# Kernel tuning notes

Hardware: AMD Instinct MI355X
Metric: run time of the kernel (lower is better)

Reference implementation:

```python
import jax, jax.numpy as jnp
import numpy as np

B, K, N, F_IN, F_OUT, T = 8, 3, 2048, 16, 64, 12


def setup_inputs() -> dict:
    key = jax.random.key(0)
    k1, k2, k3, k4 = jax.random.split(key, 4)
    x = jax.random.normal(k1, (B, N, F_IN, T), dtype=jnp.float32)
    spatial_attention = jax.random.normal(k2, (B, K, N, N), dtype=jnp.float32)
    adj = jax.random.uniform(k3, (N, N), dtype=jnp.float32)  # fusiongraph() output
    Theta = jax.random.normal(k4, (K, F_IN, F_OUT), dtype=jnp.float32) * 0.1
    return {"x": x, "spatial_attention": spatial_attention, "adj": adj, "Theta": Theta}


def _cheb_polynomials(L_tilde, k_order):
    # NOTE: original uses ELEMENTWISE multiply in the recurrence (L_tilde * T_{k-1}),
    # faithfully reproduced here.
    n = L_tilde.shape[0]
    polys = [jnp.eye(n, dtype=L_tilde.dtype), L_tilde]
    for _ in range(2, k_order):
        polys.append(2.0 * L_tilde * polys[-1] - polys[-2])
    return jnp.stack(polys[:k_order], axis=0)  # (K, N, N)


def reference(x, spatial_attention, adj, Theta):
    # Unnormalized graph Laplacian L = D - A (torch_geometric get_laplacian default).
    deg = jnp.sum(adj, axis=1)                      # (N,)
    L_tilde = jnp.diag(deg) - adj                   # (N, N)
    cheb = _cheb_polynomials(L_tilde, K)            # (K, N, N)

    # softmax over dim=1 of each (B,N,N) slice -> axis=2 of (B,K,N,N); time-invariant.
    attn = jax.nn.softmax(spatial_attention, axis=2)  # (B, K, N, N)
    Tka = cheb[None, :, :, :] * attn                  # (B, K, N, N)

    # rhs[b,n,f,t] = sum_m Tka[b,k,m,n] * x[b,m,f,t]; out = rhs @ Theta_k, summed over k.
    out = jnp.einsum('bkmn,bmft,kfo->bnot', Tka, x, Theta)  # (B, N, F_OUT, T)
    return jax.nn.relu(out)
```

## Files before the change

### kernel.cpp

```cpp
#include <hip/hip_runtime.h>


#define NB 8
#define NN 2048
#define FT 192
#define BN 64
#define BM 64
#define LBM 72

typedef __attribute__((ext_vector_type(8))) short short8;
typedef __attribute__((ext_vector_type(4))) float f32x4;

__device__ __forceinline__ unsigned short bf16_rne(float f) {
  unsigned u = __float_as_uint(f);
  u += 0x7FFFu + ((u >> 16) & 1u);
  return (unsigned short)(u >> 16);
}

__device__ __forceinline__ void gload_lds16(const float* g, float* l) {
  __builtin_amdgcn_global_load_lds(
      (const __attribute__((address_space(1))) void*)g,
      (__attribute__((address_space(3))) void*)l, 16, 0, 0);
}

__global__ __launch_bounds__(256) void k_deg(const float* __restrict__ adj,
                                             float* __restrict__ deg) {
  const int row = blockIdx.x;
  const float* r = adj + (size_t)row * NN;
  float s = 0.f;
  for (int j = threadIdx.x; j < NN; j += 256) s += r[j];
  for (int off = 32; off; off >>= 1) s += __shfl_down(s, off, 64);
  __shared__ float ls[4];
  if ((threadIdx.x & 63) == 0) ls[threadIdx.x >> 6] = s;
  __syncthreads();
  if (threadIdx.x == 0) deg[row] = ls[0] + ls[1] + ls[2] + ls[3];
}

__global__ __launch_bounds__(192) void k_xt(const float* __restrict__ x,
                                            unsigned short* __restrict__ xT) {
  const int b = blockIdx.y, m0 = blockIdx.x * 32, ft = threadIdx.x;
  const float* src = x + (size_t)b * NN * FT + ft;
  uint4* dst = (uint4*)(xT + ((size_t)b * FT + ft) * NN + m0);
#pragma unroll
  for (int g = 0; g < 4; ++g) {
    unsigned u[4];
#pragma unroll
    for (int j = 0; j < 4; ++j) {
      float lo = src[(size_t)(m0 + g * 8 + 2 * j) * FT];
      float hi = src[(size_t)(m0 + g * 8 + 2 * j + 1) * FT];
      u[j] = (unsigned)bf16_rne(lo) | ((unsigned)bf16_rne(hi) << 16);
    }
    dst[g] = make_uint4(u[0], u[1], u[2], u[3]);
  }
}

__global__ __launch_bounds__(256) void k_z0(const float* __restrict__ Sall,
                                            float* __restrict__ z0P,
                                            float* __restrict__ diagE) {
  __shared__ float zs[16][64];
  const int n0 = blockIdx.x * 64, b = blockIdx.y, half = blockIdx.z;
  const int t = threadIdx.x, n4 = (t & 15) * 4, rg = t >> 4;
  const float* S0 = Sall + (size_t)b * 3 * NN * NN;
  float z0 = 0.f, z1 = 0.f, z2 = 0.f, z3 = 0.f;
  const int mstart = half * 1024;
#pragma unroll 4
  for (int mm = rg; mm < 1024; mm += 16) {
    const int m = mstart + mm;
    const float4 v = *(const float4*)(S0 + (size_t)m * NN + n0 + n4);
    const float e0 = __expf(v.x), e1 = __expf(v.y), e2 = __expf(v.z),
                e3 = __expf(v.w);
    z0 += e0; z1 += e1; z2 += e2; z3 += e3;
    const int d = m - (n0 + n4);
    if (d >= 0 && d < 4) {
      const float ee[4] = {e0, e1, e2, e3};
      diagE[b * NN + m] = ee[d];
    }
  }
  zs[rg][n4 + 0] = z0;
  zs[rg][n4 + 1] = z1;
  zs[rg][n4 + 2] = z2;
  zs[rg][n4 + 3] = z3;
  __syncthreads();
  if (t < 64) {
    float s = 0.f;
#pragma unroll
    for (int g = 0; g < 16; ++g) s += zs[g][t];
    z0P[((size_t)b * 2 + half) * NN + n0 + t] = s;
  }
}

template <bool ISK1>
__device__ __forceinline__ void pack_chunk(const float* SrawSh,
                                           const float4 av[4],
                                           const float* __restrict__ deg,
                                           unsigned short* PtDst, float zp[4],
                                           const int pmg, const int pn4,
                                           const bool dchunk, const int n0) {
  unsigned short pk[4][4];
#pragma unroll
  for (int r = 0; r < 4; ++r) {
    const float4 s = *(const float4*)&SrawSh[(pmg * 4 + r) * BN + pn4];
    const float se[4] = {s.x, s.y, s.z, s.w};
    const float aa[4] = {av[r].x, av[r].y, av[r].z, av[r].w};
#pragma unroll
    for (int j = 0; j < 4; ++j) {
      const float e = __expf(se[j]);
      zp[j] += e;
      float cc = ISK1 ? (-aa[j]) : (2.f * aa[j] * aa[j]);
      if (dchunk) {
        if (pmg * 4 + r == pn4 + j) {
          const float L = deg[n0 + pn4 + j] - aa[j];
          cc = ISK1 ? L : (2.f * L * L - 1.f);
        }
      }
      pk[r][j] = bf16_rne(e * cc);
    }
  }
#pragma unroll
  for (int j = 0; j < 4; ++j) {
    uint2 v;
    v.x = (unsigned)pk[0][j] | ((unsigned)pk[1][j] << 16);
    v.y = (unsigned)pk[2][j] | ((unsigned)pk[3][j] << 16);
    *(uint2*)&PtDst[(pn4 + j) * LBM + pmg * 4] = v;
  }
}

template <int MS>
__global__ __launch_bounds__(256, 2) void k_main(
    const float* __restrict__ Sall, const float* __restrict__ adj,
    const float* __restrict__ deg, const unsigned short* __restrict__ xT,
    float* __restrict__ rhsP, float* __restrict__ z12P) {
  static_assert(MS == 1 || MS == 2, "MS");
  constexpr int C = 32 / MS;
  __shared__ unsigned short Pt[2][BN * LBM];
  __shared__ float Sraw[BM * BN];
  __shared__ float Zred[16][BN];

  const int flat = blockIdx.x + 32 * (blockIdx.y + 2 * blockIdx.z);
  const int xcd = flat & 7;
  const int jj = flat >> 3;
  const int tile = xcd * 4 + (jj & 3);
  const int rest = jj >> 2;
  const int kk = rest & 1;
  const int t2 = rest >> 1;
  const int ms = t2 % MS;
  const int b = t2 / MS;

  const int n0 = tile * BN, mbase = ms * (C * BM);
  const int t = threadIdx.x, lane = t & 63, w = t >> 6;
  const int ln = lane & 15, quad = lane >> 4;
  const int pn4 = (t & 15) * 4, pmg = t >> 4;
  const float* S = Sall + (size_t)(b * 3 + 1 + kk) * NN * NN;
  const unsigned short* xb = xT + (size_t)b * FT * NN;

  const f32x4 zero4 = {0.f, 0.f, 0.f, 0.f};
  f32x4 acc[4][3];
#pragma unroll
  for (int i = 0; i < 4; ++i)
#pragma unroll
    for (int q = 0; q < 3; ++q) acc[i][q] = zero4;
  float zp[4] = {0.f, 0.f, 0.f, 0.f};

  const int srow = (w << 4) + (lane >> 4);
  const int scol = (lane & 15) << 2;
  float* const lbase = &Sraw[(w << 4) * BN];

  {
    const float* g = S + (size_t)(mbase + srow) * NN + n0 + scol;
#pragma unroll
    for (int j2 = 0; j2 < 4; ++j2)
      gload_lds16(g + (size_t)(j2 * 4) * NN, lbase + j2 * 4 * BN);
  }
  float4 av[4];
#pragma unroll
  for (int r = 0; r < 4; ++r)
    av[r] = *(const float4*)(adj + (size_t)(mbase + pmg * 4 + r) * NN + n0 + pn4);
  asm volatile("s_waitcnt vmcnt(0)" ::: "memory");
  __builtin_amdgcn_sched_barrier(0);
  if (kk == 0)
    pack_chunk<true>(Sraw, av, deg, Pt[0], zp, pmg, pn4, mbase == n0, n0);
  else
    pack_chunk<false>(Sraw, av, deg, Pt[0], zp, pmg, pn4, mbase == n0, n0);
  __syncthreads();

  for (int c = 0; c < C; ++c) {
    const int cur = c & 1;
    const bool more = (c + 1 < C);
    const int m0 = mbase + c * BM;

    short8 bfr[2][3];
#pragma unroll
    for (int ks2 = 0; ks2 < 2; ++ks2)
#pragma unroll
      for (int q = 0; q < 3; ++q)
        bfr[ks2][q] = *(const short8*)(xb + (size_t)(w * 48 + q * 16 + ln) * NN +
                                       m0 + ks2 * 32 + quad * 8);
    __builtin_amdgcn_sched_barrier(0);

    if (more) {
      const int mn = m0 + BM;
      const float* g = S + (size_t)(mn + srow) * NN + n0 + scol;
#pragma unroll
      for (int j2 = 0; j2 < 4; ++j2)
        gload_lds16(g + (size_t)(j2 * 4) * NN, lbase + j2 * 4 * BN);
#pragma unroll
      for (int r = 0; r < 4; ++r)
        av[r] =
            *(const float4*)(adj + (size_t)(mn + pmg * 4 + r) * NN + n0 + pn4);
    }
    __builtin_amdgcn_sched_barrier(0);

#pragma unroll
    for (int ks2 = 0; ks2 < 2; ++ks2) {
      short8 af[4];
#pragma unroll
      for (int i = 0; i < 4; ++i)
        af[i] = *(const short8*)&Pt[cur][(i * 16 + ln) * LBM + ks2 * 32 +
                                         quad * 8];
#pragma unroll
      for (int i = 0; i < 4; ++i)
#pragma unroll
        for (int q = 0; q < 3; ++q)
          acc[i][q] = __builtin_amdgcn_mfma_f32_16x16x32_bf16(
              af[i], bfr[ks2][q], acc[i][q], 0, 0, 0);
    }

    if (more) {
      asm volatile("s_waitcnt vmcnt(0)" ::: "memory");
      __builtin_amdgcn_sched_barrier(0);
      const bool dch = (m0 + BM == n0);
      if (kk == 0)
        pack_chunk<true>(Sraw, av, deg, Pt[cur ^ 1], zp, pmg, pn4, dch, n0);
      else
        pack_chunk<false>(Sraw, av, deg, Pt[cur ^ 1], zp, pmg, pn4, dch, n0);
    }
    __syncthreads();
  }

#pragma unroll
  for (int j = 0; j < 4; ++j) Zred[pmg][pn4 + j] = zp[j];
  __syncthreads();
  if (t < 64) {
    float Z = 0.f;
#pragma unroll
    for (int g = 0; g < 16; ++g) Z += Zred[g][t];
    z12P[((size_t)(kk * 8 + b) * MS + ms) * NN + n0 + t] = Z;
  }

  float* outp = rhsP + (((size_t)(kk * 8 + b) * MS + ms) * NN + n0) * FT;
#pragma unroll
  for (int i = 0; i < 4; ++i)
#pragma unroll
    for (int q = 0; q < 3; ++q) {
      const int ft = w * 48 + q * 16 + ln;
#pragma unroll
      for (int r = 0; r < 4; ++r) {
        const int nl = i * 16 + quad * 4 + r;
        outp[(size_t)nl * FT + ft] = acc[i][q][r];
      }
    }
}

__global__ __launch_bounds__(256) void k_out(
    const float* __restrict__ x, const float* __restrict__ Theta,
    const float* __restrict__ rhsP, const float* __restrict__ z12P,
    const float* __restrict__ z0P, const float* __restrict__ diagE,
    float* __restrict__ out, int MS) {
  __shared__ float xs[4][FT], r1s[4][FT], r2s[4][FT];
  __shared__ float sc[3][4];
  const int b = blockIdx.y, n0 = blockIdx.x * 4;
  const int t = threadIdx.x, o = t & 63, nl = t >> 6;

  for (int l = t; l < 576; l += 256) {
    const int arr = l / 192, idx = l - arr * 192;
    const int row = idx / 48, c4 = (idx % 48) * 4;
    if (arr == 0) {
      *(float4*)&xs[row][c4] =
          *(const float4*)(x + ((size_t)b * NN + n0 + row) * FT + c4);
    } else {
      float4 s = {0.f, 0.f, 0.f, 0.f};
      for (int ms = 0; ms < MS; ++ms) {
        const float4 v = *(const float4*)(rhsP +
            (((size_t)((arr - 1) * 8 + b) * MS + ms) * NN + n0 + row) * FT +
            c4);
        s.x += v.x; s.y += v.y; s.z += v.z; s.w += v.w;
      }
      float* dstbase = (arr == 1) ? &r1s[0][0] : &r2s[0][0];
      *(float4*)(dstbase + row * FT + c4) = s;
    }
  }
  if (t < 12) {
    const int j = t & 3, which = t >> 2;
    float v;
    if (which < 2) {
      float z = 0.f;
      for (int ms = 0; ms < MS; ++ms)
        z += z12P[((size_t)(which * 8 + b) * MS + ms) * NN + n0 + j];
      v = 1.f / z;
    } else {
      float z = 0.f;
      for (int q = 0; q < 2; ++q) z += z0P[((size_t)b * 2 + q) * NN + n0 + j];
      v = diagE[b * NN + n0 + j] / z;
    }
    sc[which][j] = v;
  }
  __syncthreads();

  float a0[12], a1[12], a2[12];
#pragma unroll
  for (int tt = 0; tt < 12; ++tt) a0[tt] = a1[tt] = a2[tt] = 0.f;
#pragma unroll
  for (int f = 0; f < 16; ++f) {
    const float th0 = Theta[(0 * 16 + f) * 64 + o];
    const float th1 = Theta[(1 * 16 + f) * 64 + o];
    const float th2 = Theta[(2 * 16 + f) * 64 + o];
#pragma unroll
    for (int tt = 0; tt < 12; ++tt) {
      a0[tt] += th0 * xs[nl][f * 12 + tt];
      a1[tt] += th1 * r1s[nl][f * 12 + tt];
      a2[tt] += th2 * r2s[nl][f * 12 + tt];
    }
  }
  const float rz1 = sc[0][nl], rz2 = sc[1][nl], c0 = sc[2][nl];
  float r[12];
#pragma unroll
  for (int tt = 0; tt < 12; ++tt)
    r[tt] = fmaxf(a0[tt] * c0 + a1[tt] * rz1 + a2[tt] * rz2, 0.f);
  float4* op4 = (float4*)(out + (((size_t)b * NN + n0 + nl) * 64 + o) * 12);
  op4[0] = make_float4(r[0], r[1], r[2], r[3]);
  op4[1] = make_float4(r[4], r[5], r[6], r[7]);
  op4[2] = make_float4(r[8], r[9], r[10], r[11]);
}

extern "C" void kernel_launch(void* const* d_in, const int* in_sizes, int n_in,
                              void* d_out, int out_size, void* d_ws,
                              size_t ws_size, hipStream_t stream) {
  const float* x = (const float*)d_in[0];
  const float* s_attn = (const float*)d_in[1];
  const float* adj = (const float*)d_in[2];
  const float* Theta = (const float*)d_in[3];
  float* out = (float*)d_out;
  char* ws = (char*)d_ws;

  const size_t szXT = (size_t)NB * FT * NN * 2;
  const size_t szDeg = NN * 4;
  const size_t szZ0 = (size_t)NB * 2 * NN * 4;
  const size_t szDiag = (size_t)NB * NN * 4;
  const size_t base = szXT + szDeg + szZ0 + szDiag;
  const size_t perMS = (size_t)2 * NB * NN * 4
                       + (size_t)2 * NB * NN * FT * 4;

  int MS = 0;
  if (ws_size >= base + 2 * perMS) MS = 2;
  else if (ws_size >= base + 1 * perMS) MS = 1;
  if (MS == 0) return;

  unsigned short* xT = (unsigned short*)ws;
  float* deg = (float*)(ws + szXT);
  float* z0P = (float*)(ws + szXT + szDeg);
  float* diagE = (float*)(ws + szXT + szDeg + szZ0);
  float* z12P = (float*)(ws + base);
  float* rhsP = (float*)(ws + base + (size_t)2 * NB * MS * NN * 4);

  hipLaunchKernelGGL(k_deg, dim3(NN), dim3(256), 0, stream, adj, deg);
  hipLaunchKernelGGL(k_xt, dim3(64, NB), dim3(192), 0, stream, x, xT);
  hipLaunchKernelGGL(k_z0, dim3(32, NB, 2), dim3(256), 0, stream, s_attn, z0P,
                     diagE);
  if (MS == 2) {
    hipLaunchKernelGGL(k_main<2>, dim3(32, 2, NB * 2), dim3(256), 0, stream,
                       s_attn, adj, deg, xT, rhsP, z12P);
  } else {
    hipLaunchKernelGGL(k_main<1>, dim3(32, 2, NB * 1), dim3(256), 0, stream,
                       s_attn, adj, deg, xT, rhsP, z12P);
  }
  hipLaunchKernelGGL(k_out, dim3(512, NB), dim3(256), 0, stream, x, Theta,
                     rhsP, z12P, z0P, diagE, out, MS);
}
```

Before: 654.7 us.

## Fuse softmax-normalizer, both Chebyshev GEMMs and Theta epilogue into one kernel

Merges k_z0, k_main (both k=1 and k=2 branches, no M-split) and k_out into a single kernel per (batch, 32-column tile). Each block streams all three attention slices, computes the column softmax sums and diagonal term inline, runs two MFMA accumulations sharing the x fragments, and applies Theta, scaling and ReLU from LDS. This removes the partial rhs/z round trips through global memory, two launches and a redundant reread of x fragments. In exchange the grid shrinks to 512 blocks with a halved N tile, using more LDS per block and a serial full-M loop, which may lower occupancy and parallelism.

```diff
diff --git a/kernel.cpp b/kernel.cpp
--- a/kernel.cpp
+++ b/kernel.cpp
@@ -4,9 +4,10 @@
 #define NB 8
 #define NN 2048
 #define FT 192
-#define BN 64
+#define BN 32
 #define BM 64
 #define LBM 72
+#define ZST 33
 
 typedef __attribute__((ext_vector_type(8))) short short8;
 typedef __attribute__((ext_vector_type(4))) float f32x4;
@@ -54,287 +55,266 @@
   }
 }
 
-__global__ __launch_bounds__(256) void k_z0(const float* __restrict__ Sall,
-                                            float* __restrict__ z0P,
-                                            float* __restrict__ diagE) {
-  __shared__ float zs[16][64];
-  const int n0 = blockIdx.x * 64, b = blockIdx.y, half = blockIdx.z;
-  const int t = threadIdx.x, n4 = (t & 15) * 4, rg = t >> 4;
-  const float* S0 = Sall + (size_t)b * 3 * NN * NN;
-  float z0 = 0.f, z1 = 0.f, z2 = 0.f, z3 = 0.f;
-  const int mstart = half * 1024;
-#pragma unroll 4
-  for (int mm = rg; mm < 1024; mm += 16) {
-    const int m = mstart + mm;
-    const float4 v = *(const float4*)(S0 + (size_t)m * NN + n0 + n4);
-    const float e0 = __expf(v.x), e1 = __expf(v.y), e2 = __expf(v.z),
-                e3 = __expf(v.w);
-    z0 += e0; z1 += e1; z2 += e2; z3 += e3;
-    const int d = m - (n0 + n4);
-    if (d >= 0 && d < 4) {
-      const float ee[4] = {e0, e1, e2, e3};
-      diagE[b * NN + m] = ee[d];
-    }
-  }
-  zs[rg][n4 + 0] = z0;
-  zs[rg][n4 + 1] = z1;
-  zs[rg][n4 + 2] = z2;
-  zs[rg][n4 + 3] = z3;
-  __syncthreads();
-  if (t < 64) {
-    float s = 0.f;
-#pragma unroll
-    for (int g = 0; g < 16; ++g) s += zs[g][t];
-    z0P[((size_t)b * 2 + half) * NN + n0 + t] = s;
-  }
-}
-
-template <bool ISK1>
-__device__ __forceinline__ void pack_chunk(const float* SrawSh,
-                                           const float4 av[4],
-                                           const float* __restrict__ deg,
-                                           unsigned short* PtDst, float zp[4],
-                                           const int pmg, const int pn4,
-                                           const bool dchunk, const int n0) {
-  unsigned short pk[4][4];
-#pragma unroll
-  for (int r = 0; r < 4; ++r) {
-    const float4 s = *(const float4*)&SrawSh[(pmg * 4 + r) * BN + pn4];
-    const float se[4] = {s.x, s.y, s.z, s.w};
-    const float aa[4] = {av[r].x, av[r].y, av[r].z, av[r].w};
-#pragma unroll
-    for (int j = 0; j < 4; ++j) {
-      const float e = __expf(se[j]);
-      zp[j] += e;
-      float cc = ISK1 ? (-aa[j]) : (2.f * aa[j] * aa[j]);
-      if (dchunk) {
-        if (pmg * 4 + r == pn4 + j) {
-          const float L = deg[n0 + pn4 + j] - aa[j];
-          cc = ISK1 ? L : (2.f * L * L - 1.f);
-        }
-      }
-      pk[r][j] = bf16_rne(e * cc);
-    }
-  }
-#pragma unroll
-  for (int j = 0; j < 4; ++j) {
-    uint2 v;
-    v.x = (unsigned)pk[0][j] | ((unsigned)pk[1][j] << 16);
-    v.y = (unsigned)pk[2][j] | ((unsigned)pk[3][j] << 16);
-    *(uint2*)&PtDst[(pn4 + j) * LBM + pmg * 4] = v;
-  }
-}
-
-template <int MS>
-__global__ __launch_bounds__(256, 2) void k_main(
+__global__ __launch_bounds__(256, 2) void k_fused(
     const float* __restrict__ Sall, const float* __restrict__ adj,
     const float* __restrict__ deg, const unsigned short* __restrict__ xT,
-    float* __restrict__ rhsP, float* __restrict__ z12P) {
-  static_assert(MS == 1 || MS == 2, "MS");
-  constexpr int C = 32 / MS;
-  __shared__ unsigned short Pt[2][BN * LBM];
-  __shared__ float Sraw[BM * BN];
-  __shared__ float Zred[16][BN];
-
-  const int flat = blockIdx.x + 32 * (blockIdx.y + 2 * blockIdx.z);
-  const int xcd = flat & 7;
-  const int jj = flat >> 3;
-  const int tile = xcd * 4 + (jj & 3);
-  const int rest = jj >> 2;
-  const int kk = rest & 1;
-  const int t2 = rest >> 1;
-  const int ms = t2 % MS;
-  const int b = t2 / MS;
-
-  const int n0 = tile * BN, mbase = ms * (C * BM);
-  const int t = threadIdx.x, lane = t & 63, w = t >> 6;
+    const float* __restrict__ x, const float* __restrict__ Theta,
+    float* __restrict__ out) {
+  __shared__ __align__(16) char smem[74752];
+  __shared__ float dEs[BN];
+  __shared__ float sc[3][BN];
+
+  float* const Sr1 = (float*)smem;
+  float* const Sr2 = (float*)(smem + 8192);
+  unsigned short* const PtB = (unsigned short*)(smem + 16384);
+
+  const int flat = blockIdx.x + (blockIdx.y << 6);
+  const int b = flat & 7;
+  const int tile = flat >> 3;
+  const int n0 = tile * BN;
+
+  const int t = threadIdx.x;
+  const int lane = t & 63, w = t >> 6;
   const int ln = lane & 15, quad = lane >> 4;
-  const int pn4 = (t & 15) * 4, pmg = t >> 4;
-  const float* S = Sall + (size_t)(b * 3 + 1 + kk) * NN * NN;
+  const int col4 = (t & 7) << 2;
+  const int rowg = t >> 3;
+  const int srow = lane >> 3;
+  const int scol = (lane & 7) << 2;
+
+  const float* S0 = Sall + (size_t)b * 3 * NN * NN;
+  const float* S1 = S0 + (size_t)NN * NN;
+  const float* S2 = S1 + (size_t)NN * NN;
   const unsigned short* xb = xT + (size_t)b * FT * NN;
 
+  const int cdiag = n0 >> 6;
+  const float4 dgv = *(const float4*)(deg + n0 + col4);
+
   const f32x4 zero4 = {0.f, 0.f, 0.f, 0.f};
-  f32x4 acc[4][3];
-#pragma unroll
-  for (int i = 0; i < 4; ++i)
-#pragma unroll
-    for (int q = 0; q < 3; ++q) acc[i][q] = zero4;
-  float zp[4] = {0.f, 0.f, 0.f, 0.f};
-
-  const int srow = (w << 4) + (lane >> 4);
-  const int scol = (lane & 15) << 2;
-  float* const lbase = &Sraw[(w << 4) * BN];
-
+  f32x4 acc1[2][3], acc2[2][3];
+#pragma unroll
+  for (int i = 0; i < 2; ++i)
+#pragma unroll
+    for (int q = 0; q < 3; ++q) {
+      acc1[i][q] = zero4;
+      acc2[i][q] = zero4;
+    }
+  float zp0[4] = {0.f, 0.f, 0.f, 0.f};
+  float zp1[4] = {0.f, 0.f, 0.f, 0.f};
+  float zp2[4] = {0.f, 0.f, 0.f, 0.f};
+
+  auto STAGE = [&](int c) {
+    const int m0s = c * BM;
+#pragma unroll
+    for (int j2 = 0; j2 < 2; ++j2) {
+      const int r0 = (w << 4) + (j2 << 3);
+      const size_t go = (size_t)(m0s + r0 + srow) * NN + n0 + scol;
+      gload_lds16(S1 + go, Sr1 + r0 * BN);
+      gload_lds16(S2 + go, Sr2 + r0 * BN);
+    }
+  };
+
+  auto LOADAV = [&](int c, float4 av[2], float4 sv[2]) {
+#pragma unroll
+    for (int r = 0; r < 2; ++r) {
+      const int gm = c * BM + rowg * 2 + r;
+      av[r] = *(const float4*)(adj + (size_t)gm * NN + n0 + col4);
+      sv[r] = *(const float4*)(S0 + (size_t)gm * NN + n0 + col4);
+    }
+  };
+
+  auto PACK = [&](int c, int buf, const float4 av[2], const float4 sv[2]) {
+    const bool isd = (c == cdiag);
+    unsigned short* P1 = PtB + (size_t)buf * 2304;
+    unsigned short* P2 = PtB + (size_t)(2 + buf) * 2304;
+    unsigned short q1[2][4], q2[2][4];
+    const float dg[4] = {dgv.x, dgv.y, dgv.z, dgv.w};
+#pragma unroll
+    for (int r = 0; r < 2; ++r) {
+      const int lrow = rowg * 2 + r;
+      const float4 s1 = *(const float4*)&Sr1[lrow * BN + col4];
+      const float4 s2 = *(const float4*)&Sr2[lrow * BN + col4];
+      const float se1[4] = {s1.x, s1.y, s1.z, s1.w};
+      const float se2[4] = {s2.x, s2.y, s2.z, s2.w};
+      const float aa[4] = {av[r].x, av[r].y, av[r].z, av[r].w};
+      const float s0e[4] = {sv[r].x, sv[r].y, sv[r].z, sv[r].w};
+#pragma unroll
+      for (int j = 0; j < 4; ++j) {
+        const float e0 = __expf(s0e[j]);
+        const float e1 = __expf(se1[j]);
+        const float e2 = __expf(se2[j]);
+        zp0[j] += e0;
+        zp1[j] += e1;
+        zp2[j] += e2;
+        float c1 = -aa[j];
+        float c2 = 2.f * aa[j] * aa[j];
+        if (isd) {
+          if (c * BM + lrow == n0 + col4 + j) {
+            const float L = dg[j] - aa[j];
+            c1 = L;
+            c2 = 2.f * L * L - 1.f;
+            dEs[col4 + j] = e0;
+          }
+        }
+        q1[r][j] = bf16_rne(e1 * c1);
+        q2[r][j] = bf16_rne(e2 * c2);
+      }
+    }
+#pragma unroll
+    for (int j = 0; j < 4; ++j) {
+      const unsigned v1 = (unsigned)q1[0][j] | ((unsigned)q1[1][j] << 16);
+      const unsigned v2 = (unsigned)q2[0][j] | ((unsigned)q2[1][j] << 16);
+      *(unsigned*)&P1[(col4 + j) * LBM + rowg * 2] = v1;
+      *(unsigned*)&P2[(col4 + j) * LBM + rowg * 2] = v2;
+    }
+  };
+
+  STAGE(0);
   {
-    const float* g = S + (size_t)(mbase + srow) * NN + n0 + scol;
-#pragma unroll
-    for (int j2 = 0; j2 < 4; ++j2)
-      gload_lds16(g + (size_t)(j2 * 4) * NN, lbase + j2 * 4 * BN);
-  }
-  float4 av[4];
-#pragma unroll
-  for (int r = 0; r < 4; ++r)
-    av[r] = *(const float4*)(adj + (size_t)(mbase + pmg * 4 + r) * NN + n0 + pn4);
-  asm volatile("s_waitcnt vmcnt(0)" ::: "memory");
-  __builtin_amdgcn_sched_barrier(0);
-  if (kk == 0)
-    pack_chunk<true>(Sraw, av, deg, Pt[0], zp, pmg, pn4, mbase == n0, n0);
-  else
-    pack_chunk<false>(Sraw, av, deg, Pt[0], zp, pmg, pn4, mbase == n0, n0);
-  __syncthreads();
-
-  for (int c = 0; c < C; ++c) {
-    const int cur = c & 1;
-    const bool more = (c + 1 < C);
-    const int m0 = mbase + c * BM;
+    float4 av[2], sv[2];
+    LOADAV(0, av, sv);
+    asm volatile("s_waitcnt vmcnt(0)" ::: "memory");
+    __builtin_amdgcn_sched_barrier(0);
+    PACK(0, 0, av, sv);
+  }
+  __syncthreads();
+
+  for (int c = 0; c < 32; ++c) {
+    const int buf = c & 1;
+    const bool more = (c < 31);
+    const int m0 = c * BM;
 
     short8 bfr[2][3];
 #pragma unroll
     for (int ks2 = 0; ks2 < 2; ++ks2)
 #pragma unroll
       for (int q = 0; q < 3; ++q)
-        bfr[ks2][q] = *(const short8*)(xb + (size_t)(w * 48 + q * 16 + ln) * NN +
-                                       m0 + ks2 * 32 + quad * 8);
+        bfr[ks2][q] = *(const short8*)(xb +
+            (size_t)(w * 48 + q * 16 + ln) * NN + m0 + ks2 * 32 + quad * 8);
     __builtin_amdgcn_sched_barrier(0);
 
+    float4 avn[2], svn[2];
     if (more) {
-      const int mn = m0 + BM;
-      const float* g = S + (size_t)(mn + srow) * NN + n0 + scol;
-#pragma unroll
-      for (int j2 = 0; j2 < 4; ++j2)
-        gload_lds16(g + (size_t)(j2 * 4) * NN, lbase + j2 * 4 * BN);
-#pragma unroll
-      for (int r = 0; r < 4; ++r)
-        av[r] =
-            *(const float4*)(adj + (size_t)(mn + pmg * 4 + r) * NN + n0 + pn4);
+      STAGE(c + 1);
+      LOADAV(c + 1, avn, svn);
     }
     __builtin_amdgcn_sched_barrier(0);
 
 #pragma unroll
     for (int ks2 = 0; ks2 < 2; ++ks2) {
-      short8 af[4];
-#pragma unroll
-      for (int i = 0; i < 4; ++i)
-        af[i] = *(const short8*)&Pt[cur][(i * 16 + ln) * LBM + ks2 * 32 +
-                                         quad * 8];
-#pragma unroll
-      for (int i = 0; i < 4; ++i)
-#pragma unroll
-        for (int q = 0; q < 3; ++q)
-          acc[i][q] = __builtin_amdgcn_mfma_f32_16x16x32_bf16(
-              af[i], bfr[ks2][q], acc[i][q], 0, 0, 0);
+      short8 a1[2], a2[2];
+#pragma unroll
+      for (int i = 0; i < 2; ++i) {
+        a1[i] = *(const short8*)&PtB[(size_t)buf * 2304 + (i * 16 + ln) * LBM +
+                                     ks2 * 32 + quad * 8];
+        a2[i] = *(const short8*)&PtB[(size_t)(2 + buf) * 2304 +
+                                     (i * 16 + ln) * LBM + ks2 * 32 + quad * 8];
+      }
+#pragma unroll
+      for (int i = 0; i < 2; ++i)
+#pragma unroll
+        for (int q = 0; q < 3; ++q) {
+          acc1[i][q] = __builtin_amdgcn_mfma_f32_16x16x32_bf16(
+              a1[i], bfr[ks2][q], acc1[i][q], 0, 0, 0);
+          acc2[i][q] = __builtin_amdgcn_mfma_f32_16x16x32_bf16(
+              a2[i], bfr[ks2][q], acc2[i][q], 0, 0, 0);
+        }
     }
 
     if (more) {
       asm volatile("s_waitcnt vmcnt(0)" ::: "memory");
       __builtin_amdgcn_sched_barrier(0);
-      const bool dch = (m0 + BM == n0);
-      if (kk == 0)
-        pack_chunk<true>(Sraw, av, deg, Pt[cur ^ 1], zp, pmg, pn4, dch, n0);
-      else
-        pack_chunk<false>(Sraw, av, deg, Pt[cur ^ 1], zp, pmg, pn4, dch, n0);
+      PACK(c + 1, buf ^ 1, avn, svn);
     }
     __syncthreads();
   }
 
-#pragma unroll
-  for (int j = 0; j < 4; ++j) Zred[pmg][pn4 + j] = zp[j];
-  __syncthreads();
-  if (t < 64) {
+  float* Zr = (float*)smem;
+#pragma unroll
+  for (int j = 0; j < 4; ++j) {
+    Zr[0 * 32 * ZST + rowg * ZST + col4 + j] = zp0[j];
+    Zr[1 * 32 * ZST + rowg * ZST + col4 + j] = zp1[j];
+    Zr[2 * 32 * ZST + rowg * ZST + col4 + j] = zp2[j];
+  }
+  __syncthreads();
+  if (t < 96) {
+    const int which = t >> 5, n = t & 31;
     float Z = 0.f;
 #pragma unroll
-    for (int g = 0; g < 16; ++g) Z += Zred[g][t];
-    z12P[((size_t)(kk * 8 + b) * MS + ms) * NN + n0 + t] = Z;
-  }
-
-  float* outp = rhsP + (((size_t)(kk * 8 + b) * MS + ms) * NN + n0) * FT;
-#pragma unroll
-  for (int i = 0; i < 4; ++i)
+    for (int g = 0; g < 32; ++g) Z += Zr[which * 32 * ZST + g * ZST + n];
+    sc[which][n] = (which == 0) ? (dEs[n] / Z) : (1.f / Z);
+  }
+  __syncthreads();
+
+  float* const r1s = (float*)smem;
+  float* const r2s = (float*)(smem + 25088);
+  float* const xs = (float*)(smem + 50176);
+#pragma unroll
+  for (int i = 0; i < 2; ++i)
 #pragma unroll
     for (int q = 0; q < 3; ++q) {
       const int ft = w * 48 + q * 16 + ln;
 #pragma unroll
       for (int r = 0; r < 4; ++r) {
         const int nl = i * 16 + quad * 4 + r;
-        outp[(size_t)nl * FT + ft] = acc[i][q][r];
+        r1s[nl * 196 + ft] = acc1[i][q][r];
+        r2s[nl * 196 + ft] = acc2[i][q][r];
       }
     }
-}
-
-__global__ __launch_bounds__(256) void k_out(
-    const float* __restrict__ x, const float* __restrict__ Theta,
-    const float* __restrict__ rhsP, const float* __restrict__ z12P,
-    const float* __restrict__ z0P, const float* __restrict__ diagE,
-    float* __restrict__ out, int MS) {
-  __shared__ float xs[4][FT], r1s[4][FT], r2s[4][FT];
-  __shared__ float sc[3][4];
-  const int b = blockIdx.y, n0 = blockIdx.x * 4;
-  const int t = threadIdx.x, o = t & 63, nl = t >> 6;
-
-  for (int l = t; l < 576; l += 256) {
-    const int arr = l / 192, idx = l - arr * 192;
-    const int row = idx / 48, c4 = (idx % 48) * 4;
-    if (arr == 0) {
-      *(float4*)&xs[row][c4] =
-          *(const float4*)(x + ((size_t)b * NN + n0 + row) * FT + c4);
-    } else {
-      float4 s = {0.f, 0.f, 0.f, 0.f};
-      for (int ms = 0; ms < MS; ++ms) {
-        const float4 v = *(const float4*)(rhsP +
-            (((size_t)((arr - 1) * 8 + b) * MS + ms) * NN + n0 + row) * FT +
-            c4);
-        s.x += v.x; s.y += v.y; s.z += v.z; s.w += v.w;
-      }
-      float* dstbase = (arr == 1) ? &r1s[0][0] : &r2s[0][0];
-      *(float4*)(dstbase + row * FT + c4) = s;
-    }
-  }
-  if (t < 12) {
-    const int j = t & 3, which = t >> 2;
-    float v;
-    if (which < 2) {
-      float z = 0.f;
-      for (int ms = 0; ms < MS; ++ms)
-        z += z12P[((size_t)(which * 8 + b) * MS + ms) * NN + n0 + j];
-      v = 1.f / z;
-    } else {
-      float z = 0.f;
-      for (int q = 0; q < 2; ++q) z += z0P[((size_t)b * 2 + q) * NN + n0 + j];
-      v = diagE[b * NN + n0 + j] / z;
-    }
-    sc[which][j] = v;
-  }
-  __syncthreads();
-
-  float a0[12], a1[12], a2[12];
-#pragma unroll
-  for (int tt = 0; tt < 12; ++tt) a0[tt] = a1[tt] = a2[tt] = 0.f;
+  for (int l = t; l < 32 * 48; l += 256) {
+    const int row = l / 48, c4 = (l % 48) * 4;
+    *(float4*)&xs[row * 192 + c4] =
+        *(const float4*)(x + ((size_t)b * NN + n0 + row) * FT + c4);
+  }
+  __syncthreads();
+
+  const int o = t & 63, nl2 = t >> 6;
+  float th0[16], th1[16], th2[16];
 #pragma unroll
   for (int f = 0; f < 16; ++f) {
-    const float th0 = Theta[(0 * 16 + f) * 64 + o];
-    const float th1 = Theta[(1 * 16 + f) * 64 + o];
-    const float th2 = Theta[(2 * 16 + f) * 64 + o];
-#pragma unroll
-    for (int tt = 0; tt < 12; ++tt) {
-      a0[tt] += th0 * xs[nl][f * 12 + tt];
-      a1[tt] += th1 * r1s[nl][f * 12 + tt];
-      a2[tt] += th2 * r2s[nl][f * 12 + tt];
-    }
-  }
-  const float rz1 = sc[0][nl], rz2 = sc[1][nl], c0 = sc[2][nl];
-  float r[12];
-#pragma unroll
-  for (int tt = 0; tt < 12; ++tt)
-    r[tt] = fmaxf(a0[tt] * c0 + a1[tt] * rz1 + a2[tt] * rz2, 0.f);
-  float4* op4 = (float4*)(out + (((size_t)b * NN + n0 + nl) * 64 + o) * 12);
-  op4[0] = make_float4(r[0], r[1], r[2], r[3]);
-  op4[1] = make_float4(r[4], r[5], r[6], r[7]);
-  op4[2] = make_float4(r[8], r[9], r[10], r[11]);
+    th0[f] = Theta[f * 64 + o];
+    th1[f] = Theta[(16 + f) * 64 + o];
+    th2[f] = Theta[(32 + f) * 64 + o];
+  }
+#pragma unroll 1
+  for (int ni = 0; ni < 8; ++ni) {
+    const int n = ni * 4 + nl2;
+    float a0[12], a1[12], a2[12];
+#pragma unroll
+    for (int e = 0; e < 12; ++e) a0[e] = a1[e] = a2[e] = 0.f;
+#pragma unroll
+    for (int f = 0; f < 16; ++f) {
+      const f32x4* xv = (const f32x4*)&xs[n * 192 + f * 12];
+      const f32x4* r1v = (const f32x4*)&r1s[n * 196 + f * 12];
+      const f32x4* r2v = (const f32x4*)&r2s[n * 196 + f * 12];
+#pragma unroll
+      for (int g = 0; g < 3; ++g)
+#pragma unroll
+        for (int e = 0; e < 4; ++e) {
+          a0[g * 4 + e] += th0[f] * xv[g][e];
+          a1[g * 4 + e] += th1[f] * r1v[g][e];
+          a2[g * 4 + e] += th2[f] * r2v[g][e];
+        }
+    }
+    const float c0 = sc[0][n], rz1 = sc[1][n], rz2 = sc[2][n];
+    float4* op = (float4*)(out + (((size_t)b * NN + n0 + n) * 64 + o) * 12);
+#pragma unroll
+    for (int g = 0; g < 3; ++g) {
+      float4 rv;
+      rv.x = fmaxf(a0[g * 4 + 0] * c0 + a1[g * 4 + 0] * rz1 + a2[g * 4 + 0] * rz2, 0.f);
+      rv.y = fmaxf(a0[g * 4 + 1] * c0 + a1[g * 4 + 1] * rz1 + a2[g * 4 + 1] * rz2, 0.f);
+      rv.z = fmaxf(a0[g * 4 + 2] * c0 + a1[g * 4 + 2] * rz1 + a2[g * 4 + 2] * rz2, 0.f);
+      rv.w = fmaxf(a0[g * 4 + 3] * c0 + a1[g * 4 + 3] * rz1 + a2[g * 4 + 3] * rz2, 0.f);
+      op[g] = rv;
+    }
+  }
 }
 
 extern "C" void kernel_launch(void* const* d_in, const int* in_sizes, int n_in,
                               void* d_out, int out_size, void* d_ws,
                               size_t ws_size, hipStream_t stream) {
+  (void)in_sizes;
+  (void)n_in;
+  (void)out_size;
   const float* x = (const float*)d_in[0];
   const float* s_attn = (const float*)d_in[1];
   const float* adj = (const float*)d_in[2];
@@ -344,35 +324,13 @@
 
   const size_t szXT = (size_t)NB * FT * NN * 2;
   const size_t szDeg = NN * 4;
-  const size_t szZ0 = (size_t)NB * 2 * NN * 4;
-  const size_t szDiag = (size_t)NB * NN * 4;
-  const size_t base = szXT + szDeg + szZ0 + szDiag;
-  const size_t perMS = (size_t)2 * NB * NN * 4
-                       + (size_t)2 * NB * NN * FT * 4;
-
-  int MS = 0;
-  if (ws_size >= base + 2 * perMS) MS = 2;
-  else if (ws_size >= base + 1 * perMS) MS = 1;
-  if (MS == 0) return;
+  if (ws_size < szXT + szDeg) return;
 
   unsigned short* xT = (unsigned short*)ws;
   float* deg = (float*)(ws + szXT);
-  float* z0P = (float*)(ws + szXT + szDeg);
-  float* diagE = (float*)(ws + szXT + szDeg + szZ0);
-  float* z12P = (float*)(ws + base);
-  float* rhsP = (float*)(ws + base + (size_t)2 * NB * MS * NN * 4);
 
   hipLaunchKernelGGL(k_deg, dim3(NN), dim3(256), 0, stream, adj, deg);
   hipLaunchKernelGGL(k_xt, dim3(64, NB), dim3(192), 0, stream, x, xT);
-  hipLaunchKernelGGL(k_z0, dim3(32, NB, 2), dim3(256), 0, stream, s_attn, z0P,
-                     diagE);
-  if (MS == 2) {
-    hipLaunchKernelGGL(k_main<2>, dim3(32, 2, NB * 2), dim3(256), 0, stream,
-                       s_attn, adj, deg, xT, rhsP, z12P);
-  } else {
-    hipLaunchKernelGGL(k_main<1>, dim3(32, 2, NB * 1), dim3(256), 0, stream,
-                       s_attn, adj, deg, xT, rhsP, z12P);
-  }
-  hipLaunchKernelGGL(k_out, dim3(512, NB), dim3(256), 0, stream, x, Theta,
-                     rhsP, z12P, z0P, diagE, out, MS);
-}
+  hipLaunchKernelGGL(k_fused, dim3(64, NB), dim3(256), 0, stream, s_attn, adj,
+                     deg, xT, x, Theta, out);
+}
```

New measurement: 642.8 us. No clear change (-1.8%).
